# Kernel optimization log

Measured on AMD Instinct MI355X. Metric: run time of the kernel, lower is better.

The kernel has to match this reference:

```python
import jax, jax.numpy as jnp
import numpy as np

R = 65  # num_relations


def rgcn_conv(x, edge_index, edge_type, W, root, bias):
    """PyG RGCNConv with per-relation mean aggregation.
    Aggregate-then-transform (linearity lets us swap the order):
      mean_r[n] = mean over edges e with type r, dst(e)=n of x[src(e)]
      out = sum_r mean_r @ W_r + x @ root + bias
    """
    N = x.shape[0]
    src, dst = edge_index[0], edge_index[1]
    seg = edge_type * N + dst  # composite (relation, dst) segment id
    sums = jax.ops.segment_sum(x[src], seg, num_segments=R * N)
    sums = sums.reshape(R, N, -1)  # [R, N, F]
    cnt = jax.ops.segment_sum(jnp.ones(src.shape, x.dtype), seg, num_segments=R * N)
    cnt = cnt.reshape(R, N, 1)
    mean = sums / jnp.maximum(cnt, 1.0)
    return jnp.einsum('rni,rio->no', mean, W) + x @ root + bias


def setup_inputs() -> dict:
    key = jax.random.key(0)
    ks = jax.random.split(key, 20)
    N, E, F_in, H, M = 8000, 192000, 64, 256, 64
    B = 128
    inp = {
        'x': jax.random.normal(ks[0], (N, F_in), jnp.float32),
        'edge_index': jax.random.randint(ks[1], (2, E), 0, N),
        'edge_type': jax.random.randint(ks[2], (E,), 0, R),
        'batch': jnp.sort(jax.random.randint(ks[3], (N,), 0, B)),
    }
    def glorot(k, shape):
        fan = shape[-2] + shape[-1]
        return jax.random.normal(k, shape, jnp.float32) * jnp.sqrt(2.0 / fan)
    inp['W1'] = glorot(ks[4], (R, F_in, H)); inp['root1'] = glorot(ks[5], (F_in, H)); inp['b1'] = jnp.zeros((H,), jnp.float32)
    inp['W2'] = glorot(ks[6], (R, H, H));   inp['root2'] = glorot(ks[7], (H, H));   inp['b2'] = jnp.zeros((H,), jnp.float32)
    inp['W3'] = glorot(ks[8], (R, H, H));   inp['root3'] = glorot(ks[9], (H, H));   inp['b3'] = jnp.zeros((H,), jnp.float32)
    inp['ws_w'] = glorot(ks[10], (H, 1));    inp['ws_b'] = jnp.zeros((1,), jnp.float32)
    inp['m_w1'] = glorot(ks[11], (H, M)); inp['m_b1'] = jnp.zeros((M,), jnp.float32)
    inp['m_w2'] = glorot(ks[12], (M, M)); inp['m_b2'] = jnp.zeros((M,), jnp.float32)
    inp['m_w3'] = glorot(ks[13], (M, 1)); inp['m_b3'] = jnp.zeros((1,), jnp.float32)
    return inp


def reference(x, edge_index, edge_type, batch,
              W1, root1, b1, W2, root2, b2, W3, root3, b3,
              ws_w, ws_b, m_w1, m_b1, m_w2, m_b2, m_w3, m_b3):
    B = 128  # number of graphs in the batch
    h = jax.nn.relu(rgcn_conv(x, edge_index, edge_type, W1, root1, b1))
    h = jax.nn.relu(rgcn_conv(h, edge_index, edge_type, W2, root2, b2))
    h = jax.nn.relu(rgcn_conv(h, edge_index, edge_type, W3, root3, b3))
    # WeightedSum pooling: sigmoid gate per node, scatter-sum per graph
    w = jax.nn.sigmoid(h @ ws_w + ws_b)            # [N, 1]
    pooled = jax.ops.segment_sum(w * h, batch, num_segments=B)  # [B, H]
    # MLP head
    m = jax.nn.relu(pooled @ m_w1 + m_b1)
    m = jax.nn.relu(m @ m_w2 + m_b2)
    return m @ m_w3 + m_b3                          # [B, 1]
```

## Files before the change

kernel.cpp:

```cpp
#include <hip/hip_runtime.h>

#define NNODES 8000
#define NEDGES 192000
#define NREL   65
#define RP     66
#define HDIM   256
#define FDIM   64
#define NGRAPH 128
#define MDIM   64
#define TILE_M 64
#define MAXT   3456
#define EPTOT  (NEDGES + NNODES)

typedef _Float16 half8 __attribute__((ext_vector_type(8)));
typedef _Float16 half4 __attribute__((ext_vector_type(4)));
typedef float    f32x4 __attribute__((ext_vector_type(4)));


__global__ void count_kernel(const int* __restrict__ ei, const int* __restrict__ et,
                             int* __restrict__ cnt_rn, int* __restrict__ type_cnt,
                             int* __restrict__ ddeg) {
    __shared__ int lbin[NREL];
    int tid = threadIdx.x;
    if (tid < NREL) lbin[tid] = 0;
    __syncthreads();
    int e = blockIdx.x * 256 + tid;
    if (e < NEDGES) {
        int t = et[e];
        int d = ei[NEDGES + e];
        atomicAdd(&lbin[t], 1);
        atomicAdd(&cnt_rn[t * NNODES + d], 1);
        atomicAdd(&ddeg[d], 1);
    }
    __syncthreads();
    if (tid < NREL && lbin[tid] > 0) atomicAdd(&type_cnt[tid], lbin[tid]);
}

__global__ void scan_tiles_kernel(const int* __restrict__ type_cnt, int* __restrict__ type_off,
                                  int* __restrict__ tile_rel, int* __restrict__ tile_start,
                                  int* __restrict__ tile_nrows) {
    __shared__ int s_off[RP + 1];
    __shared__ int s_toff[RP + 1];
    if (threadIdx.x == 0) {
        int off = 0, toff = 0;
        for (int r = 0; r < RP; r++) {
            int c = (r < NREL) ? type_cnt[r] : NNODES;
            s_off[r] = off; s_toff[r] = toff;
            off += c; toff += (c + TILE_M - 1) / TILE_M;
        }
        s_off[RP] = off; s_toff[RP] = toff;
        type_off[RP] = off;
    }
    __syncthreads();
    int r = threadIdx.x;
    if (r < RP) {
        type_off[r] = s_off[r];
        int c = s_off[r + 1] - s_off[r];
        int nt = (c + TILE_M - 1) / TILE_M;
        for (int i = 0; i < nt; i++) {
            int idx = s_toff[r] + i;
            tile_rel[idx]   = r;
            tile_start[idx] = s_off[r] + i * TILE_M;
            tile_nrows[idx] = min(TILE_M, c - i * TILE_M);
        }
    }
}

__global__ void dst_scan_kernel(const int* __restrict__ ddeg, int* __restrict__ dst_off) {
    __shared__ int part[256];
    int t = threadIdx.x;
    int base = t * 32;
    int s = 0;
    for (int i = 0; i < 32; i++) {
        int n = base + i;
        if (n < NNODES) s += ddeg[n] + 1;
    }
    part[t] = s;
    __syncthreads();
    if (t == 0) {
        int run = 0;
        for (int i = 0; i < 256; i++) { int tmp = part[i]; part[i] = run; run += tmp; }
        dst_off[NNODES] = run;
    }
    __syncthreads();
    int run = part[t];
    for (int i = 0; i < 32; i++) {
        int n = base + i;
        if (n < NNODES) { dst_off[n] = run; run += ddeg[n] + 1; }
    }
}

__global__ void scatter_kernel(const int* __restrict__ ei, const int* __restrict__ et,
                               const int* __restrict__ cnt_rn, const int* __restrict__ type_off,
                               int* __restrict__ type_cur,
                               const int* __restrict__ dst_off, int* __restrict__ dst_cur,
                               int* __restrict__ esrc, int* __restrict__ eq,
                               float* __restrict__ escale) {
    __shared__ int lbin[NREL];
    __shared__ int gbase[NREL];
    int tid = threadIdx.x;
    if (tid < NREL) lbin[tid] = 0;
    __syncthreads();
    int i = blockIdx.x * 256 + tid;
    int t = 0, lrank = 0;
    bool is_edge = (i < NEDGES);
    if (is_edge) {
        t = et[i];
        lrank = atomicAdd(&lbin[t], 1);
    }
    __syncthreads();
    if (tid < NREL && lbin[tid] > 0) gbase[tid] = atomicAdd(&type_cur[tid], lbin[tid]);
    __syncthreads();
    if (is_edge) {
        int d = ei[NEDGES + i];
        int p = type_off[t] + gbase[t] + lrank;
        int q = dst_off[d] + atomicAdd(&dst_cur[d], 1);
        esrc[p] = ei[i];
        eq[p] = q;
        escale[p] = 1.0f / (float)cnt_rn[t * NNODES + d];
    } else if (i < EPTOT) {
        int n = i - NEDGES;
        int p = NEDGES + n;
        int q = dst_off[n] + atomicAdd(&dst_cur[n], 1);
        esrc[p] = n; eq[p] = q; escale[p] = 1.0f;
    }
}

__global__ void convW_kernel(const float* __restrict__ W, const float* __restrict__ root,
                             _Float16* __restrict__ Wt, int K) {
    int r = blockIdx.x, k0 = blockIdx.y * 32, n0 = blockIdx.z * 32;
    const float* src = (r < NREL) ? (W + (size_t)r * K * HDIM) : root;
    __shared__ float tile[32][33];
    int tj = threadIdx.x & 31, ti = threadIdx.x >> 5;
    #pragma unroll
    for (int s = 0; s < 4; s++) {
        int i = ti + s * 8;
        tile[i][tj] = src[(size_t)(k0 + i) * HDIM + n0 + tj];
    }
    __syncthreads();
    #pragma unroll
    for (int s = 0; s < 4; s++) {
        int i = ti + s * 8;
        Wt[((size_t)r * HDIM + (n0 + i)) * K + k0 + tj] = (_Float16)tile[tj][i];
    }
}

__global__ void conv_x_kernel(const float* __restrict__ x, _Float16* __restrict__ x16) {
    int i = blockIdx.x * 256 + threadIdx.x;
    if (i < NNODES * FDIM) x16[i] = (_Float16)x[i];
}

template <int K>
__global__ __launch_bounds__(256)
void edge_gemm_kernel(const _Float16* __restrict__ hin, const _Float16* __restrict__ Wt,
                      const int* __restrict__ esrc, const int* __restrict__ eq,
                      const float* __restrict__ escale,
                      const int* __restrict__ tile_rel, const int* __restrict__ tile_start,
                      const int* __restrict__ tile_nrows,
                      _Float16* __restrict__ Y) {
    int nr = tile_nrows[blockIdx.x];
    if (nr == 0) return;
    int r  = tile_rel[blockIdx.x];
    int ts = tile_start[blockIdx.x];

    constexpr int LK = K + 8;
    constexpr int SO = HDIM + 8;
    constexpr int LMAX = (LK > SO) ? LK : SO;
    __shared__ _Float16 sbuf[TILE_M * LMAX];
    __shared__ int   sq[TILE_M];
    __shared__ float sscale[TILE_M];

    int tid = threadIdx.x;
    constexpr int CPR = K / 8;
    for (int idx = tid; idx < TILE_M * CPR; idx += 256) {
        int row = idx / CPR, c = idx % CPR;
        uint4 v = make_uint4(0, 0, 0, 0);
        if (row < nr) {
            int src = esrc[ts + row];
            v = *(const uint4*)(hin + (size_t)src * K + c * 8);
        }
        *(uint4*)&sbuf[row * LK + c * 8] = v;
    }
    if (tid < TILE_M) {
        if (tid < nr) { sq[tid] = eq[ts + tid]; sscale[tid] = escale[ts + tid]; }
        else          { sq[tid] = 0;            sscale[tid] = 0.f; }
    }
    __syncthreads();

    int lane = tid & 63, w = tid >> 6;
    int lm = lane & 15, quad = lane >> 4;
    f32x4 acc[4][4] = {};
    const _Float16* Bbase = Wt + ((size_t)r * HDIM + w * 64 + lm) * K + quad * 8;
    const _Float16* Abase = sbuf + lm * LK + quad * 8;

    for (int kk = 0; kk < K; kk += 32) {
        half8 a[4], b[4];
        #pragma unroll
        for (int mt = 0; mt < 4; mt++)
            a[mt] = *(const half8*)(Abase + mt * 16 * LK + kk);
        #pragma unroll
        for (int nt = 0; nt < 4; nt++)
            b[nt] = *(const half8*)(Bbase + nt * 16 * K + kk);
        #pragma unroll
        for (int mt = 0; mt < 4; mt++)
            #pragma unroll
            for (int nt = 0; nt < 4; nt++)
                acc[mt][nt] = __builtin_amdgcn_mfma_f32_16x16x32_f16(a[mt], b[nt], acc[mt][nt], 0, 0, 0);
    }

    __syncthreads();

    #pragma unroll
    for (int mt = 0; mt < 4; mt++) {
        #pragma unroll
        for (int rr = 0; rr < 4; rr++) {
            int row = mt * 16 + quad * 4 + rr;
            float s = sscale[row];
            #pragma unroll
            for (int nt = 0; nt < 4; nt++) {
                int col = w * 64 + nt * 16 + lm;
                sbuf[row * SO + col] = (_Float16)(acc[mt][nt][rr] * s);
            }
        }
    }
    __syncthreads();

    for (int idx = tid; idx < TILE_M * 32; idx += 256) {
        int row = idx >> 5, seg = idx & 31;
        if (row < nr) {
            uint4 v = *(const uint4*)&sbuf[row * SO + seg * 8];
            *(uint4*)(Y + (size_t)sq[row] * HDIM + seg * 8) = v;
        }
    }
}

__global__ __launch_bounds__(256)
void reduce_kernel(const _Float16* __restrict__ Y, const int* __restrict__ dst_off,
                   const float* __restrict__ bias, _Float16* __restrict__ hout) {
    int n = blockIdx.x;
    int start = dst_off[n], end = dst_off[n + 1];
    int t = threadIdx.x;
    int c = t & 31;
    int r = t >> 5;
    float acc[8] = {0, 0, 0, 0, 0, 0, 0, 0};
    for (int j = start + r; j < end; j += 8) {
        half8 v = *(const half8*)(Y + (size_t)j * HDIM + c * 8);
        #pragma unroll
        for (int k = 0; k < 8; k++) acc[k] += (float)v[k];
    }
    __shared__ float red[8][32][8];
    #pragma unroll
    for (int k = 0; k < 8; k++) red[r][c][k] = acc[k];
    __syncthreads();
    if (t < 32) {
        float a[8];
        #pragma unroll
        for (int k = 0; k < 8; k++) a[k] = red[0][t][k];
        for (int rr = 1; rr < 8; rr++)
            #pragma unroll
            for (int k = 0; k < 8; k++) a[k] += red[rr][t][k];
        half8 o;
        #pragma unroll
        for (int k = 0; k < 8; k++) {
            float v = a[k] + bias[t * 8 + k];
            o[k] = (_Float16)(v > 0.f ? v : 0.f);
        }
        *(half8*)(hout + (size_t)n * HDIM + t * 8) = o;
    }
}


__global__ void gate_kernel(const _Float16* __restrict__ h, const float* __restrict__ ws_w,
                            const float* __restrict__ ws_b, float* __restrict__ gate) {
    int node = blockIdx.x * 4 + (threadIdx.x >> 6);
    int lane = threadIdx.x & 63;
    half4 v = *(const half4*)(h + (size_t)node * HDIM + lane * 4);
    float s = 0.f;
    #pragma unroll
    for (int k = 0; k < 4; k++) s += (float)v[k] * ws_w[lane * 4 + k];
    for (int o = 32; o > 0; o >>= 1) s += __shfl_down(s, o, 64);
    if (lane == 0) gate[node] = 1.f / (1.f + __expf(-(s + ws_b[0])));
}

__global__ void pool_kernel(const _Float16* __restrict__ h, const float* __restrict__ gate,
                            const int* __restrict__ batch, float* __restrict__ pooled) {
    int g = blockIdx.x, t = threadIdx.x;
    int a = 0, b = NNODES;
    while (a < b) { int m = (a + b) >> 1; if (batch[m] < g) a = m + 1; else b = m; }
    int lo = a;
    b = NNODES;
    while (a < b) { int m = (a + b) >> 1; if (batch[m] < g + 1) a = m + 1; else b = m; }
    int hi = a;
    float acc = 0.f;
    for (int n = lo; n < hi; n++)
        acc += gate[n] * (float)h[(size_t)n * HDIM + t];
    pooled[(size_t)g * HDIM + t] = acc;
}

__global__ void head_kernel(const float* __restrict__ pooled,
                            const float* __restrict__ w1, const float* __restrict__ b1,
                            const float* __restrict__ w2, const float* __restrict__ b2,
                            const float* __restrict__ w3, const float* __restrict__ b3,
                            float* __restrict__ out) {
    int b = blockIdx.x, tid = threadIdx.x;
    __shared__ float sp[HDIM];
    __shared__ float m1[MDIM];
    __shared__ float m2[MDIM];
    for (int i = tid; i < HDIM; i += 64) sp[i] = pooled[(size_t)b * HDIM + i];
    __syncthreads();
    float a = b1[tid];
    for (int i = 0; i < HDIM; i++) a += sp[i] * w1[i * MDIM + tid];
    m1[tid] = a > 0.f ? a : 0.f;
    __syncthreads();
    float c = b2[tid];
    for (int i = 0; i < MDIM; i++) c += m1[i] * w2[i * MDIM + tid];
    m2[tid] = c > 0.f ? c : 0.f;
    __syncthreads();
    float p = m2[tid] * w3[tid];
    for (int o = 32; o > 0; o >>= 1) p += __shfl_down(p, o, 64);
    if (tid == 0) out[b] = p + b3[0];
}


extern "C" void kernel_launch(void* const* d_in, const int* in_sizes, int n_in,
                              void* d_out, int out_size, void* d_ws, size_t ws_size,
                              hipStream_t stream) {
    const float* x     = (const float*)d_in[0];
    const int*   ei    = (const int*)d_in[1];
    const int*   et    = (const int*)d_in[2];
    const int*   batch = (const int*)d_in[3];
    const float* W1    = (const float*)d_in[4];
    const float* root1 = (const float*)d_in[5];
    const float* b1    = (const float*)d_in[6];
    const float* W2    = (const float*)d_in[7];
    const float* root2 = (const float*)d_in[8];
    const float* b2    = (const float*)d_in[9];
    const float* W3    = (const float*)d_in[10];
    const float* root3 = (const float*)d_in[11];
    const float* b3    = (const float*)d_in[12];
    const float* ws_w  = (const float*)d_in[13];
    const float* ws_b  = (const float*)d_in[14];
    const float* m_w1  = (const float*)d_in[15];
    const float* m_b1  = (const float*)d_in[16];
    const float* m_w2  = (const float*)d_in[17];
    const float* m_b2  = (const float*)d_in[18];
    const float* m_w3  = (const float*)d_in[19];
    const float* m_b3  = (const float*)d_in[20];
    float* out = (float*)d_out;

    char* ws = (char*)d_ws;
    size_t o = 0;
    auto take = [&](size_t bytes) { size_t r = o; o = (o + bytes + 255) & ~(size_t)255; return r; };

    size_t o_cnt_rn = take((size_t)NREL * NNODES * 4);
    size_t o_tcnt   = take(RP * 4);
    size_t o_tcur   = take(RP * 4);
    size_t o_toff   = take((RP + 1) * 4);
    size_t o_ddeg   = take((size_t)NNODES * 4);
    size_t o_dcur   = take((size_t)NNODES * 4);
    size_t o_doff   = take((size_t)(NNODES + 1) * 4);
    size_t o_esrc   = take((size_t)EPTOT * 4);
    size_t o_eq     = take((size_t)EPTOT * 4);
    size_t o_escale = take((size_t)EPTOT * 4);
    size_t o_trel   = take(MAXT * 4);
    size_t o_tstart = take(MAXT * 4);
    size_t o_tnrows = take(MAXT * 4);
    size_t o_wt1    = take((size_t)RP * HDIM * FDIM * 2);
    size_t o_wt2    = take((size_t)RP * HDIM * HDIM * 2);
    size_t o_wt3    = take((size_t)RP * HDIM * HDIM * 2);
    size_t o_x16    = take((size_t)NNODES * FDIM * 2);
    size_t o_h16    = take((size_t)NNODES * HDIM * 2);
    size_t o_gate   = take((size_t)NNODES * 4);
    size_t o_pool   = take((size_t)NGRAPH * HDIM * 4);
    size_t o_y16    = take((size_t)EPTOT * HDIM * 2);

    int*      cnt_rn   = (int*)(ws + o_cnt_rn);
    int*      type_cnt = (int*)(ws + o_tcnt);
    int*      type_cur = (int*)(ws + o_tcur);
    int*      type_off = (int*)(ws + o_toff);
    int*      ddeg     = (int*)(ws + o_ddeg);
    int*      dst_cur  = (int*)(ws + o_dcur);
    int*      dst_off  = (int*)(ws + o_doff);
    int*      esrc     = (int*)(ws + o_esrc);
    int*      eq       = (int*)(ws + o_eq);
    float*    escale   = (float*)(ws + o_escale);
    int*      trel     = (int*)(ws + o_trel);
    int*      tstart   = (int*)(ws + o_tstart);
    int*      tnrows   = (int*)(ws + o_tnrows);
    _Float16* Wt1      = (_Float16*)(ws + o_wt1);
    _Float16* Wt2      = (_Float16*)(ws + o_wt2);
    _Float16* Wt3      = (_Float16*)(ws + o_wt3);
    _Float16* x16      = (_Float16*)(ws + o_x16);
    _Float16* h16      = (_Float16*)(ws + o_h16);
    float*    gate     = (float*)(ws + o_gate);
    float*    pooled   = (float*)(ws + o_pool);
    _Float16* Y16      = (_Float16*)(ws + o_y16);

    hipMemsetAsync(ws + o_cnt_rn, 0, o_toff - o_cnt_rn, stream);
    hipMemsetAsync(ws + o_ddeg, 0, o_doff - o_ddeg, stream);
    hipMemsetAsync(ws + o_tnrows, 0, MAXT * 4, stream);

    count_kernel<<<(NEDGES + 255) / 256, 256, 0, stream>>>(ei, et, cnt_rn, type_cnt, ddeg);
    scan_tiles_kernel<<<1, 128, 0, stream>>>(type_cnt, type_off, trel, tstart, tnrows);
    dst_scan_kernel<<<1, 256, 0, stream>>>(ddeg, dst_off);
    scatter_kernel<<<(EPTOT + 255) / 256, 256, 0, stream>>>(ei, et, cnt_rn, type_off, type_cur,
                                                            dst_off, dst_cur, esrc, eq, escale);

    convW_kernel<<<dim3(RP, FDIM / 32, HDIM / 32), 256, 0, stream>>>(W1, root1, Wt1, FDIM);
    convW_kernel<<<dim3(RP, HDIM / 32, HDIM / 32), 256, 0, stream>>>(W2, root2, Wt2, HDIM);
    convW_kernel<<<dim3(RP, HDIM / 32, HDIM / 32), 256, 0, stream>>>(W3, root3, Wt3, HDIM);
    conv_x_kernel<<<(NNODES * FDIM + 255) / 256, 256, 0, stream>>>(x, x16);

    edge_gemm_kernel<FDIM><<<MAXT, 256, 0, stream>>>(x16, Wt1, esrc, eq, escale,
                                                     trel, tstart, tnrows, Y16);
    reduce_kernel<<<NNODES, 256, 0, stream>>>(Y16, dst_off, b1, h16);

    edge_gemm_kernel<HDIM><<<MAXT, 256, 0, stream>>>(h16, Wt2, esrc, eq, escale,
                                                     trel, tstart, tnrows, Y16);
    reduce_kernel<<<NNODES, 256, 0, stream>>>(Y16, dst_off, b2, h16);

    edge_gemm_kernel<HDIM><<<MAXT, 256, 0, stream>>>(h16, Wt3, esrc, eq, escale,
                                                     trel, tstart, tnrows, Y16);
    reduce_kernel<<<NNODES, 256, 0, stream>>>(Y16, dst_off, b3, h16);

    gate_kernel<<<NNODES / 4, 256, 0, stream>>>(h16, ws_w, ws_b, gate);
    pool_kernel<<<NGRAPH, 256, 0, stream>>>(h16, gate, batch, pooled);
    head_kernel<<<NGRAPH, 64, 0, stream>>>(pooled, m_w1, m_b1, m_w2, m_b2, m_w3, m_b3, out);

    (void)in_sizes; (void)n_in; (void)out_size; (void)ws_size;
}
```

Baseline: 491.2 us.

## Split edge GEMM K staging, fuse weight conversions, gate, and pool/head kernels

Merges the three weight-transpose launches into one grid and folds the sigmoid gate into the last reduce kernel. It also fuses pooling with the MLP head, removing several launches and one global round trip. Separately, the edge GEMM now stages its gathered A rows in two K halves and writes output in two column passes, shrinking shared memory per block to raise occupancy. The cost is extra barriers and a second gather pass inside the GEMM.

Result: slower. 519.1 us (+5.7%).

```diff
diff --git a/kernel.cpp b/kernel.cpp
--- a/kernel.cpp
+++ b/kernel.cpp
@@ -11,6 +11,7 @@
 #define TILE_M 64
 #define MAXT   3456
 #define EPTOT  (NEDGES + NNODES)
+
 
 typedef _Float16 half8 __attribute__((ext_vector_type(8)));
 typedef _Float16 half4 __attribute__((ext_vector_type(4)));
@@ -126,9 +127,16 @@
     }
 }
 
-__global__ void convW_kernel(const float* __restrict__ W, const float* __restrict__ root,
-                             _Float16* __restrict__ Wt, int K) {
-    int r = blockIdx.x, k0 = blockIdx.y * 32, n0 = blockIdx.z * 32;
+__global__ void convW_all_kernel(const float* __restrict__ W1, const float* __restrict__ root1,
+                                 const float* __restrict__ W2, const float* __restrict__ root2,
+                                 const float* __restrict__ W3, const float* __restrict__ root3,
+                                 _Float16* __restrict__ Wt1, _Float16* __restrict__ Wt2,
+                                 _Float16* __restrict__ Wt3) {
+    int r = blockIdx.x, y = blockIdx.y, n0 = blockIdx.z * 32;
+    const float *W, *root; _Float16* Wt; int K, k0;
+    if (y < 2)       { W = W1; root = root1; Wt = Wt1; K = FDIM; k0 = y * 32; }
+    else if (y < 10) { W = W2; root = root2; Wt = Wt2; K = HDIM; k0 = (y - 2) * 32; }
+    else             { W = W3; root = root3; Wt = Wt3; K = HDIM; k0 = (y - 10) * 32; }
     const float* src = (r < NREL) ? (W + (size_t)r * K * HDIM) : root;
     __shared__ float tile[32][33];
     int tj = threadIdx.x & 31, ti = threadIdx.x >> 5;
@@ -163,27 +171,26 @@
     int r  = tile_rel[blockIdx.x];
     int ts = tile_start[blockIdx.x];
 
-    constexpr int LK = K + 8;
-    constexpr int SO = HDIM + 8;
-    constexpr int LMAX = (LK > SO) ? LK : SO;
-    __shared__ _Float16 sbuf[TILE_M * LMAX];
+    constexpr int KH = (K > 128) ? 128 : K;
+    constexpr int NH = K / KH;
+    constexpr int LK = KH + 8;
+    constexpr int SO = 136;
+    constexpr int LSZ = (LK > SO) ? LK : SO;
+    __shared__ _Float16 sbuf[TILE_M * LSZ];
+    __shared__ int   ssrc[TILE_M];
     __shared__ int   sq[TILE_M];
     __shared__ float sscale[TILE_M];
 
     int tid = threadIdx.x;
-    constexpr int CPR = K / 8;
-    for (int idx = tid; idx < TILE_M * CPR; idx += 256) {
-        int row = idx / CPR, c = idx % CPR;
-        uint4 v = make_uint4(0, 0, 0, 0);
-        if (row < nr) {
-            int src = esrc[ts + row];
-            v = *(const uint4*)(hin + (size_t)src * K + c * 8);
-        }
-        *(uint4*)&sbuf[row * LK + c * 8] = v;
-    }
     if (tid < TILE_M) {
-        if (tid < nr) { sq[tid] = eq[ts + tid]; sscale[tid] = escale[ts + tid]; }
-        else          { sq[tid] = 0;            sscale[tid] = 0.f; }
+        if (tid < nr) {
+            ssrc[tid] = esrc[ts + tid];
+            sq[tid] = eq[ts + tid];
+            sscale[tid] = escale[ts + tid];
+        } else {
+            ssrc[tid] = esrc[ts];
+            sq[tid] = 0; sscale[tid] = 0.f;
+        }
     }
     __syncthreads();
 
@@ -193,50 +200,66 @@
     const _Float16* Bbase = Wt + ((size_t)r * HDIM + w * 64 + lm) * K + quad * 8;
     const _Float16* Abase = sbuf + lm * LK + quad * 8;
 
-    for (int kk = 0; kk < K; kk += 32) {
-        half8 a[4], b[4];
+    constexpr int CPR = KH / 8;
+    for (int h = 0; h < NH; h++) {
+        for (int idx = tid; idx < TILE_M * CPR; idx += 256) {
+            int row = idx / CPR, c = idx % CPR;
+            uint4 v = *(const uint4*)(hin + (size_t)ssrc[row] * K + h * KH + c * 8);
+            *(uint4*)&sbuf[row * LK + c * 8] = v;
+        }
+        __syncthreads();
         #pragma unroll
-        for (int mt = 0; mt < 4; mt++)
-            a[mt] = *(const half8*)(Abase + mt * 16 * LK + kk);
-        #pragma unroll
-        for (int nt = 0; nt < 4; nt++)
-            b[nt] = *(const half8*)(Bbase + nt * 16 * K + kk);
-        #pragma unroll
-        for (int mt = 0; mt < 4; mt++)
+        for (int kk = 0; kk < KH; kk += 32) {
+            half8 a[4], b[4];
+            #pragma unroll
+            for (int mt = 0; mt < 4; mt++)
+                a[mt] = *(const half8*)(Abase + mt * 16 * LK + kk);
             #pragma unroll
             for (int nt = 0; nt < 4; nt++)
-                acc[mt][nt] = __builtin_amdgcn_mfma_f32_16x16x32_f16(a[mt], b[nt], acc[mt][nt], 0, 0, 0);
-    }
-
-    __syncthreads();
+                b[nt] = *(const half8*)(Bbase + nt * 16 * K + h * KH + kk);
+            #pragma unroll
+            for (int mt = 0; mt < 4; mt++)
+                #pragma unroll
+                for (int nt = 0; nt < 4; nt++)
+                    acc[mt][nt] = __builtin_amdgcn_mfma_f32_16x16x32_f16(a[mt], b[nt], acc[mt][nt], 0, 0, 0);
+        }
+        __syncthreads();
+    }
 
     #pragma unroll
-    for (int mt = 0; mt < 4; mt++) {
-        #pragma unroll
-        for (int rr = 0; rr < 4; rr++) {
-            int row = mt * 16 + quad * 4 + rr;
-            float s = sscale[row];
+    for (int p = 0; p < 2; p++) {
+        if (p) __syncthreads();
+        if ((w >> 1) == p) {
             #pragma unroll
-            for (int nt = 0; nt < 4; nt++) {
-                int col = w * 64 + nt * 16 + lm;
-                sbuf[row * SO + col] = (_Float16)(acc[mt][nt][rr] * s);
+            for (int mt = 0; mt < 4; mt++) {
+                #pragma unroll
+                for (int rr = 0; rr < 4; rr++) {
+                    int row = mt * 16 + quad * 4 + rr;
+                    float s = sscale[row];
+                    #pragma unroll
+                    for (int nt = 0; nt < 4; nt++) {
+                        int col = (w & 1) * 64 + nt * 16 + lm;
+                        sbuf[row * SO + col] = (_Float16)(acc[mt][nt][rr] * s);
+                    }
+                }
             }
         }
-    }
-    __syncthreads();
-
-    for (int idx = tid; idx < TILE_M * 32; idx += 256) {
-        int row = idx >> 5, seg = idx & 31;
-        if (row < nr) {
-            uint4 v = *(const uint4*)&sbuf[row * SO + seg * 8];
-            *(uint4*)(Y + (size_t)sq[row] * HDIM + seg * 8) = v;
+        __syncthreads();
+        for (int idx = tid; idx < TILE_M * 16; idx += 256) {
+            int row = idx >> 4, seg = idx & 15;
+            if (row < nr) {
+                uint4 v = *(const uint4*)&sbuf[row * SO + seg * 8];
+                *(uint4*)(Y + (size_t)sq[row] * HDIM + p * 128 + seg * 8) = v;
+            }
         }
     }
 }
 
 __global__ __launch_bounds__(256)
 void reduce_kernel(const _Float16* __restrict__ Y, const int* __restrict__ dst_off,
-                   const float* __restrict__ bias, _Float16* __restrict__ hout) {
+                   const float* __restrict__ bias, _Float16* __restrict__ hout,
+                   const float* __restrict__ ws_w, const float* __restrict__ ws_b,
+                   float* __restrict__ gate) {
     int n = blockIdx.x;
     int start = dst_off[n], end = dst_off[n + 1];
     int t = threadIdx.x;
@@ -260,30 +283,28 @@
             #pragma unroll
             for (int k = 0; k < 8; k++) a[k] += red[rr][t][k];
         half8 o;
+        float g = 0.f;
         #pragma unroll
         for (int k = 0; k < 8; k++) {
             float v = a[k] + bias[t * 8 + k];
-            o[k] = (_Float16)(v > 0.f ? v : 0.f);
+            v = v > 0.f ? v : 0.f;
+            o[k] = (_Float16)v;
+            if (gate) g += v * ws_w[t * 8 + k];
         }
         *(half8*)(hout + (size_t)n * HDIM + t * 8) = o;
-    }
-}
-
-
-__global__ void gate_kernel(const _Float16* __restrict__ h, const float* __restrict__ ws_w,
-                            const float* __restrict__ ws_b, float* __restrict__ gate) {
-    int node = blockIdx.x * 4 + (threadIdx.x >> 6);
-    int lane = threadIdx.x & 63;
-    half4 v = *(const half4*)(h + (size_t)node * HDIM + lane * 4);
-    float s = 0.f;
-    #pragma unroll
-    for (int k = 0; k < 4; k++) s += (float)v[k] * ws_w[lane * 4 + k];
-    for (int o = 32; o > 0; o >>= 1) s += __shfl_down(s, o, 64);
-    if (lane == 0) gate[node] = 1.f / (1.f + __expf(-(s + ws_b[0])));
-}
-
-__global__ void pool_kernel(const _Float16* __restrict__ h, const float* __restrict__ gate,
-                            const int* __restrict__ batch, float* __restrict__ pooled) {
+        if (gate) {
+            for (int off = 16; off > 0; off >>= 1) g += __shfl_down(g, off, 32);
+            if (t == 0) gate[n] = 1.f / (1.f + __expf(-(g + ws_b[0])));
+        }
+    }
+}
+
+__global__ void pool_head_kernel(const _Float16* __restrict__ h, const float* __restrict__ gate,
+                                 const int* __restrict__ batch,
+                                 const float* __restrict__ w1, const float* __restrict__ b1,
+                                 const float* __restrict__ w2, const float* __restrict__ b2,
+                                 const float* __restrict__ w3, const float* __restrict__ b3,
+                                 float* __restrict__ out) {
     int g = blockIdx.x, t = threadIdx.x;
     int a = 0, b = NNODES;
     while (a < b) { int m = (a + b) >> 1; if (batch[m] < g) a = m + 1; else b = m; }
@@ -294,31 +315,28 @@
     float acc = 0.f;
     for (int n = lo; n < hi; n++)
         acc += gate[n] * (float)h[(size_t)n * HDIM + t];
-    pooled[(size_t)g * HDIM + t] = acc;
-}
-
-__global__ void head_kernel(const float* __restrict__ pooled,
-                            const float* __restrict__ w1, const float* __restrict__ b1,
-                            const float* __restrict__ w2, const float* __restrict__ b2,
-                            const float* __restrict__ w3, const float* __restrict__ b3,
-                            float* __restrict__ out) {
-    int b = blockIdx.x, tid = threadIdx.x;
     __shared__ float sp[HDIM];
     __shared__ float m1[MDIM];
     __shared__ float m2[MDIM];
-    for (int i = tid; i < HDIM; i += 64) sp[i] = pooled[(size_t)b * HDIM + i];
-    __syncthreads();
-    float a = b1[tid];
-    for (int i = 0; i < HDIM; i++) a += sp[i] * w1[i * MDIM + tid];
-    m1[tid] = a > 0.f ? a : 0.f;
-    __syncthreads();
-    float c = b2[tid];
-    for (int i = 0; i < MDIM; i++) c += m1[i] * w2[i * MDIM + tid];
-    m2[tid] = c > 0.f ? c : 0.f;
-    __syncthreads();
-    float p = m2[tid] * w3[tid];
-    for (int o = 32; o > 0; o >>= 1) p += __shfl_down(p, o, 64);
-    if (tid == 0) out[b] = p + b3[0];
+    sp[t] = acc;
+    __syncthreads();
+    if (t < MDIM) {
+        float v = b1[t];
+        for (int i = 0; i < HDIM; i++) v += sp[i] * w1[i * MDIM + t];
+        m1[t] = v > 0.f ? v : 0.f;
+    }
+    __syncthreads();
+    if (t < MDIM) {
+        float v = b2[t];
+        for (int i = 0; i < MDIM; i++) v += m1[i] * w2[i * MDIM + t];
+        m2[t] = v > 0.f ? v : 0.f;
+    }
+    __syncthreads();
+    if (t < 64) {
+        float p = m2[t] * w3[t];
+        for (int o = 32; o > 0; o >>= 1) p += __shfl_down(p, o, 64);
+        if (t == 0) out[g] = p + b3[0];
+    }
 }
 
 
@@ -371,7 +389,6 @@
     size_t o_x16    = take((size_t)NNODES * FDIM * 2);
     size_t o_h16    = take((size_t)NNODES * HDIM * 2);
     size_t o_gate   = take((size_t)NNODES * 4);
-    size_t o_pool   = take((size_t)NGRAPH * HDIM * 4);
     size_t o_y16    = take((size_t)EPTOT * HDIM * 2);
 
     int*      cnt_rn   = (int*)(ws + o_cnt_rn);
@@ -393,7 +410,6 @@
     _Float16* x16      = (_Float16*)(ws + o_x16);
     _Float16* h16      = (_Float16*)(ws + o_h16);
     float*    gate     = (float*)(ws + o_gate);
-    float*    pooled   = (float*)(ws + o_pool);
     _Float16* Y16      = (_Float16*)(ws + o_y16);
 
     hipMemsetAsync(ws + o_cnt_rn, 0, o_toff - o_cnt_rn, stream);
@@ -406,26 +422,24 @@
     scatter_kernel<<<(EPTOT + 255) / 256, 256, 0, stream>>>(ei, et, cnt_rn, type_off, type_cur,
                                                             dst_off, dst_cur, esrc, eq, escale);
 
-    convW_kernel<<<dim3(RP, FDIM / 32, HDIM / 32), 256, 0, stream>>>(W1, root1, Wt1, FDIM);
-    convW_kernel<<<dim3(RP, HDIM / 32, HDIM / 32), 256, 0, stream>>>(W2, root2, Wt2, HDIM);
-    convW_kernel<<<dim3(RP, HDIM / 32, HDIM / 32), 256, 0, stream>>>(W3, root3, Wt3, HDIM);
+    convW_all_kernel<<<dim3(RP, 18, HDIM / 32), 256, 0, stream>>>(W1, root1, W2, root2, W3, root3,
+                                                                  Wt1, Wt2, Wt3);
     conv_x_kernel<<<(NNODES * FDIM + 255) / 256, 256, 0, stream>>>(x, x16);
 
     edge_gemm_kernel<FDIM><<<MAXT, 256, 0, stream>>>(x16, Wt1, esrc, eq, escale,
                                                      trel, tstart, tnrows, Y16);
-    reduce_kernel<<<NNODES, 256, 0, stream>>>(Y16, dst_off, b1, h16);
+    reduce_kernel<<<NNODES, 256, 0, stream>>>(Y16, dst_off, b1, h16, ws_w, ws_b, nullptr);
 
     edge_gemm_kernel<HDIM><<<MAXT, 256, 0, stream>>>(h16, Wt2, esrc, eq, escale,
                                                      trel, tstart, tnrows, Y16);
-    reduce_kernel<<<NNODES, 256, 0, stream>>>(Y16, dst_off, b2, h16);
+    reduce_kernel<<<NNODES, 256, 0, stream>>>(Y16, dst_off, b2, h16, ws_w, ws_b, nullptr);
 
     edge_gemm_kernel<HDIM><<<MAXT, 256, 0, stream>>>(h16, Wt3, esrc, eq, escale,
                                                      trel, tstart, tnrows, Y16);
-    reduce_kernel<<<NNODES, 256, 0, stream>>>(Y16, dst_off, b3, h16);
-
-    gate_kernel<<<NNODES / 4, 256, 0, stream>>>(h16, ws_w, ws_b, gate);
-    pool_kernel<<<NGRAPH, 256, 0, stream>>>(h16, gate, batch, pooled);
-    head_kernel<<<NGRAPH, 64, 0, stream>>>(pooled, m_w1, m_b1, m_w2, m_b2, m_w3, m_b3, out);
+    reduce_kernel<<<NNODES, 256, 0, stream>>>(Y16, dst_off, b3, h16, ws_w, ws_b, gate);
+
+    pool_head_kernel<<<NGRAPH, 256, 0, stream>>>(h16, gate, batch,
+                                                 m_w1, m_b1, m_w2, m_b2, m_w3, m_b3, out);
 
     (void)in_sizes; (void)n_in; (void)out_size; (void)ws_size;
 }
```
